# Kernel optimization log

Hardware: AMD Instinct MI355X
Metric: run time of the kernel (lower is better)

Reference implementation:

```python
import jax, jax.numpy as jnp
import numpy as np

N_BINS = 15  # matches ECELoss(n_bins=15)


def setup_inputs() -> dict:
    key = jax.random.key(0)
    k1, k2 = jax.random.split(key)
    B, C = 2_097_152, 16
    logits = jax.random.normal(k1, (B, C), dtype=jnp.float32) * 2.0
    # binary multi-label targets, stored as float (forward casts to float anyway)
    targets = (jax.random.uniform(k2, (B, C)) < 0.5).astype(jnp.float32)
    return {"logits": logits, "targets": targets}


def reference(logits, targets):
    """Vectorized ECE: single bucketize + segment-sum pass replacing the
    per-class/per-bin Python loops. Same math: for each non-empty (class, bin)
    cell, accumulate |mean_conf - mean_acc| * (cell_count / B), then divide by
    the number of non-empty cells."""
    B, C = logits.shape
    probs = jax.nn.sigmoid(logits)  # [B, C]
    boundaries = jnp.linspace(0.0, 1.0, N_BINS + 1)
    # bin b satisfies boundaries[b] <= p < boundaries[b+1]  (>= start, < end)
    bin_idx = jnp.searchsorted(boundaries, probs, side="right") - 1  # [B, C]
    valid = (bin_idx >= 0) & (bin_idx < N_BINS)  # p == 1.0 falls in no bin
    seg = jnp.where(valid, jnp.arange(C)[None, :] * N_BINS + bin_idx, C * N_BINS)
    seg = seg.reshape(-1)
    num_seg = C * N_BINS + 1  # last segment = dumping ground for invalid
    ones = jnp.ones((B * C,), dtype=probs.dtype)
    cnt = jax.ops.segment_sum(ones, seg, num_segments=num_seg)[:-1]           # [C*n_bins]
    sum_p = jax.ops.segment_sum(probs.reshape(-1), seg, num_segments=num_seg)[:-1]
    sum_t = jax.ops.segment_sum(targets.reshape(-1), seg, num_segments=num_seg)[:-1]
    nonempty = cnt > 0
    safe = jnp.where(nonempty, cnt, 1.0)
    # |avg_confidence - accuracy| * mask.mean()  per non-empty cell
    term = jnp.abs(sum_p / safe - sum_t / safe) * (cnt / B)
    total = jnp.sum(jnp.where(nonempty, term, 0.0))
    count = jnp.sum(nonempty)
    return jnp.where(count > 0, total / count, jnp.zeros((), probs.dtype))
```

## Files before the change

kernel.cpp:

```cpp
#include <hip/hip_runtime.h>
#include <math.h>

#define NC 16
#define NBINS 15
#define NCELL (NC * NBINS)
#define GRID 2048
#define ITERS 64
#define BROWS 2097152.0
#define MAXREP 8

__global__ void __launch_bounds__(256, 8) ece_partial(const float* __restrict__ logits,
                                                      const float* __restrict__ targets,
                                                      float* __restrict__ ws, int nrep) {
    __shared__ unsigned int h[16 * 256];
#pragma unroll
    for (int r = 0; r < 16; ++r) h[r * 256 + threadIdx.x] = 0u;
    __syncthreads();

    const float LOG2E = 1.4426950408889634f;
    const int tid    = blockIdx.x * 256 + threadIdx.x;
    const int stride = GRID * 256;
    const int col    = threadIdx.x;

#define PROC(x, t)                                                     \
    {                                                                  \
        float e = __builtin_amdgcn_exp2f(-(x) * LOG2E);                \
        float p = __builtin_amdgcn_rcpf(1.0f + e);                     \
        int b = (int)(p * 15.0f);           \
        unsigned int pf = (unsigned int)(p * 1024.0f + 0.5f);          \
        unsigned int val = (1u << 25) | (((unsigned int)(t)) << 18) | pf; \
        h[b * 256 + col] += val;                                       \
    }

    for (int k = 0; k < ITERS; k += 4) {
        int i0 = tid + k * stride;
        int i1 = i0 + stride, i2 = i1 + stride, i3 = i2 + stride;
        float l0 = logits[i0], l1 = logits[i1], l2 = logits[i2], l3 = logits[i3];
        float t0 = targets[i0], t1 = targets[i1], t2 = targets[i2], t3 = targets[i3];
        PROC(l0, t0);
        PROC(l1, t1);
        PROC(l2, t2);
        PROC(l3, t3);
    }
#undef PROC
    __syncthreads();

    int idx = threadIdx.x;
    if (idx < NCELL) {
        int cls = idx & 15, bin = idx >> 4;
        int base = bin * 256 + cls;
        unsigned int cnt = 0, tsum = 0, psum = 0;
#pragma unroll
        for (int k = 0; k < 16; ++k) {
            unsigned int v = h[base + 16 * k];
            cnt  += v >> 25;
            tsum += (v >> 18) & 127u;
            psum += v & 0x3FFFFu;
        }
        float* r = ws + (blockIdx.x & (nrep - 1)) * (3 * NCELL);
        atomicAdd(&r[idx],             (float)cnt);
        atomicAdd(&r[NCELL + idx],     (float)psum * (1.0f / 1024.0f));
        atomicAdd(&r[2 * NCELL + idx], (float)tsum);
    }
}

__global__ void __launch_bounds__(256) ece_final(const float* __restrict__ ws,
                                                 float* __restrict__ out, int nrep) {
    __shared__ double s_term[256];
    __shared__ int s_ne[256];
    int i = threadIdx.x;
    double term = 0.0;
    int ne = 0;
    if (i < NCELL) {
        float cnt = 0.0f, sp = 0.0f, st = 0.0f;
        for (int rep = 0; rep < nrep; ++rep) {
            const float* r = ws + rep * (3 * NCELL);
            cnt += r[i];
            sp  += r[NCELL + i];
            st  += r[2 * NCELL + i];
        }
        if (cnt > 0.0f) {
            ne = 1;
            term = fabs((double)sp / (double)cnt - (double)st / (double)cnt) *
                   ((double)cnt / BROWS);
        }
    }
    s_term[i] = term;
    s_ne[i] = ne;
    __syncthreads();
    for (int off = 128; off > 0; off >>= 1) {
        if (i < off) {
            s_term[i] += s_term[i + off];
            s_ne[i]   += s_ne[i + off];
        }
        __syncthreads();
    }
    if (i == 0) out[0] = (s_ne[0] > 0) ? (float)(s_term[0] / (double)s_ne[0]) : 0.0f;
}

extern "C" void kernel_launch(void* const* d_in, const int* in_sizes, int n_in,
                              void* d_out, int out_size, void* d_ws, size_t ws_size,
                              hipStream_t stream) {
    const float* logits  = (const float*)d_in[0];
    const float* targets = (const float*)d_in[1];
    float* ws  = (float*)d_ws;
    float* out = (float*)d_out;

    int nrep = MAXREP;
    while (nrep > 1 && (size_t)(nrep * 3 * NCELL * sizeof(float)) > ws_size) nrep >>= 1;

    hipMemsetAsync(ws, 0, nrep * 3 * NCELL * sizeof(float), stream);
    ece_partial<<<GRID, 256, 0, stream>>>(logits, targets, ws, nrep);
    ece_final<<<1, 256, 0, stream>>>(ws, out, nrep);
}
```

Baseline: 280.4 us.

## Software-pipeline loads with double-buffered registers and split LDS histograms

Each block now handles a contiguous 32K-element chunk instead of grid-striding, and prefetches the next group of 8 logits and targets into registers while the current group is processed. Two separate LDS histogram copies take alternating elements, which breaks the read-modify-write dependency chain on the same slot. The grid is halved and occupancy lowered to 4 blocks per CU to make room for the larger LDS and registers. Probability precision in the packed word rises to 2048 steps, which leaves less headroom in the 18-bit probability field. Bin indices are masked to stay in range.

```diff
diff --git a/kernel.cpp b/kernel.cpp
--- a/kernel.cpp
+++ b/kernel.cpp
@@ -4,62 +4,85 @@
 #define NC 16
 #define NBINS 15
 #define NCELL (NC * NBINS)
-#define GRID 2048
-#define ITERS 64
+#define GRID 1024
+#define TPB 256
+#define BLOCK_ELEMS 32768
+#define NGROUP 16
 #define BROWS 2097152.0
 #define MAXREP 8
 
-__global__ void __launch_bounds__(256, 8) ece_partial(const float* __restrict__ logits,
+__global__ void __launch_bounds__(256, 4) ece_partial(const float* __restrict__ logits,
                                                       const float* __restrict__ targets,
                                                       float* __restrict__ ws, int nrep) {
-    __shared__ unsigned int h[16 * 256];
+    __shared__ unsigned int h[2 * 16 * 256];
 #pragma unroll
-    for (int r = 0; r < 16; ++r) h[r * 256 + threadIdx.x] = 0u;
+    for (int r = 0; r < 32; ++r) h[r * 256 + threadIdx.x] = 0u;
     __syncthreads();
 
     const float LOG2E = 1.4426950408889634f;
-    const int tid    = blockIdx.x * 256 + threadIdx.x;
-    const int stride = GRID * 256;
-    const int col    = threadIdx.x;
+    const int col  = threadIdx.x;
+    const int base = blockIdx.x * BLOCK_ELEMS + threadIdx.x;
 
-#define PROC(x, t)                                                     \
-    {                                                                  \
-        float e = __builtin_amdgcn_exp2f(-(x) * LOG2E);                \
-        float p = __builtin_amdgcn_rcpf(1.0f + e);                     \
-        int b = (int)(p * 15.0f);           \
-        unsigned int pf = (unsigned int)(p * 1024.0f + 0.5f);          \
-        unsigned int val = (1u << 25) | (((unsigned int)(t)) << 18) | pf; \
-        h[b * 256 + col] += val;                                       \
+    float cl[8], ct[8], nl[8], nt_[8];
+#pragma unroll
+    for (int j = 0; j < 8; ++j) {
+        nl[j]  = logits[base + j * TPB];
+        nt_[j] = targets[base + j * TPB];
     }
 
-    for (int k = 0; k < ITERS; k += 4) {
-        int i0 = tid + k * stride;
-        int i1 = i0 + stride, i2 = i1 + stride, i3 = i2 + stride;
-        float l0 = logits[i0], l1 = logits[i1], l2 = logits[i2], l3 = logits[i3];
-        float t0 = targets[i0], t1 = targets[i1], t2 = targets[i2], t3 = targets[i3];
-        PROC(l0, t0);
-        PROC(l1, t1);
-        PROC(l2, t2);
-        PROC(l3, t3);
+    for (int g = 0; g < NGROUP; ++g) {
+#pragma unroll
+        for (int j = 0; j < 8; ++j) { cl[j] = nl[j]; ct[j] = nt_[j]; }
+        if (g < NGROUP - 1) {
+            int it0 = (g + 1) * 8;
+#pragma unroll
+            for (int j = 0; j < 8; ++j) {
+                nl[j]  = logits[base + (it0 + j) * TPB];
+                nt_[j] = targets[base + (it0 + j) * TPB];
+            }
+        }
+#pragma unroll
+        for (int q = 0; q < 4; ++q) {
+            float x0 = cl[2 * q],     t0 = ct[2 * q];
+            float x1 = cl[2 * q + 1], t1 = ct[2 * q + 1];
+            float e0 = __builtin_amdgcn_exp2f(-x0 * LOG2E);
+            float e1 = __builtin_amdgcn_exp2f(-x1 * LOG2E);
+            float p0 = __builtin_amdgcn_rcpf(1.0f + e0);
+            float p1 = __builtin_amdgcn_rcpf(1.0f + e1);
+            int b0 = ((int)(p0 * 15.0f)) & 15;
+            int b1 = ((int)(p1 * 15.0f)) & 15;
+            unsigned int v0 = (1u << 25) | (((unsigned int)t0) << 18) |
+                              (unsigned int)(p0 * 2048.0f + 0.5f);
+            unsigned int v1 = (1u << 25) | (((unsigned int)t1) << 18) |
+                              (unsigned int)(p1 * 2048.0f + 0.5f);
+            int a0 = b0 * 256 + col;
+            int a1 = 4096 + b1 * 256 + col;
+            unsigned int u0 = h[a0];
+            unsigned int u1 = h[a1];
+            h[a0] = u0 + v0;
+            h[a1] = u1 + v1;
+        }
     }
-#undef PROC
     __syncthreads();
 
     int idx = threadIdx.x;
     if (idx < NCELL) {
         int cls = idx & 15, bin = idx >> 4;
-        int base = bin * 256 + cls;
         unsigned int cnt = 0, tsum = 0, psum = 0;
 #pragma unroll
-        for (int k = 0; k < 16; ++k) {
-            unsigned int v = h[base + 16 * k];
-            cnt  += v >> 25;
-            tsum += (v >> 18) & 127u;
-            psum += v & 0x3FFFFu;
+        for (int s = 0; s < 2; ++s) {
+            int rowb = s * 4096 + bin * 256 + cls;
+#pragma unroll
+            for (int k = 0; k < 16; ++k) {
+                unsigned int v = h[rowb + 16 * k];
+                cnt  += v >> 25;
+                tsum += (v >> 18) & 127u;
+                psum += v & 0x3FFFFu;
+            }
         }
         float* r = ws + (blockIdx.x & (nrep - 1)) * (3 * NCELL);
         atomicAdd(&r[idx],             (float)cnt);
-        atomicAdd(&r[NCELL + idx],     (float)psum * (1.0f / 1024.0f));
+        atomicAdd(&r[NCELL + idx],     (float)psum * (1.0f / 2048.0f));
         atomicAdd(&r[2 * NCELL + idx], (float)tsum);
     }
 }
@@ -110,6 +133,6 @@
     while (nrep > 1 && (size_t)(nrep * 3 * NCELL * sizeof(float)) > ws_size) nrep >>= 1;
 
     hipMemsetAsync(ws, 0, nrep * 3 * NCELL * sizeof(float), stream);
-    ece_partial<<<GRID, 256, 0, stream>>>(logits, targets, ws, nrep);
+    ece_partial<<<GRID, TPB, 0, stream>>>(logits, targets, ws, nrep);
     ece_final<<<1, 256, 0, stream>>>(ws, out, nrep);
 }
```

After: 286.0 us. About the same (+2.0%).
